# Performance work log

Measured on AMD Instinct MI355X. Metric: run time of the kernel, lower is better.

## Reference

```python
import jax, jax.numpy as jnp
import numpy as np
import math

EPS = 1e-5

def _ln(x, g, b):
    m = jnp.mean(x, axis=-1, keepdims=True)
    v = jnp.mean((x - m) ** 2, axis=-1, keepdims=True)
    return (x - m) * jax.lax.rsqrt(v + EPS) * g + b

def _heads(t, H):
    B, T, C = t.shape
    return t.reshape(B, T, H, C // H).transpose(0, 2, 1, 3)  # [B,H,T,D]

def _merge(t):
    B, H, T, D = t.shape
    return t.transpose(0, 2, 1, 3).reshape(B, T, H * D)

def _self_attn(x, w, b, pw, pb, H):
    B, T, C = x.shape
    q, k, v = jnp.split(x @ w + b, 3, axis=-1)
    q, k, v = _heads(q, H), _heads(k, H), _heads(v, H)
    D = C // H
    att = jnp.einsum('bhqd,bhkd->bhqk', q, k) * (1.0 / math.sqrt(D))
    causal = jnp.tril(jnp.ones((T, T), bool))
    att = jnp.where(causal[None, None], att, jnp.float32(-jnp.inf))
    att = jax.nn.softmax(att, axis=-1)
    out = _merge(jnp.einsum('bhqk,bhkd->bhqd', att, v))
    return out @ pw + pb

def _cross_attn(enc, dec, w, b, pw, pb, H):
    B, Td, C = dec.shape
    q_dec = jnp.split(dec @ w + b, 3, axis=-1)[0]
    _, k_enc, v_enc = jnp.split(enc @ w + b, 3, axis=-1)
    q = _heads(q_dec, H); k = _heads(k_enc, H); v = _heads(v_enc, H)
    D = C // H
    att = jnp.einsum('bhqd,bhkd->bhqk', q, k) * (1.0 / math.sqrt(D))
    att = jax.nn.softmax(att, axis=-1)
    out = _merge(jnp.einsum('bhqk,bhkd->bhqd', att, v))
    return out @ pw + pb

def _block(x, encoder_embd,
           ln1_g, ln1_b, ln2_g, ln2_b, ln3_g, ln3_b,
           attn_w, attn_b, aproj_w, aproj_b,
           ca_w, ca_b, caproj_w, caproj_b,
           fc_w, fc_b, mproj_w, mproj_b,
           down_w, down_b, up_w, up_b, H=16):
    x = x + _self_attn(_ln(x, ln1_g, ln1_b), attn_w, attn_b, aproj_w, aproj_b, H)
    x = x + _cross_attn(encoder_embd, _ln(x, ln2_g, ln2_b), ca_w, ca_b, caproj_w, caproj_b, H)
    h = jax.nn.gelu(_ln(x, ln3_g, ln3_b) @ fc_w + fc_b, approximate=True) @ mproj_w + mproj_b
    adapt = jax.nn.gelu(h @ down_w + down_b, approximate=True) @ up_w + up_b + h  # Adapter residual
    return x + adapt


def setup_inputs() -> dict:
    key = jax.random.key(0)
    ks = jax.random.split(key, 12)
    B, T, Te, C, H = 4, 1024, 257, 1024, 16
    s = 0.02
    f32 = jnp.float32
    return {
        'x': jax.random.normal(ks[0], (B, T, C), f32),
        'encoder_embd': jax.random.normal(ks[1], (B, Te, C), f32),
        'prefix_embd': jnp.zeros((B, 1, C), f32),
        'ln1_g': jnp.ones((C,), f32), 'ln1_b': jnp.zeros((C,), f32),
        'ln2_g': jnp.ones((C,), f32), 'ln2_b': jnp.zeros((C,), f32),
        'ln3_g': jnp.ones((C,), f32), 'ln3_b': jnp.zeros((C,), f32),
        'attn_w': jax.random.normal(ks[2], (C, 3 * C), f32) * s,
        'attn_b': jnp.zeros((3 * C,), f32),
        'aproj_w': jax.random.normal(ks[3], (C, C), f32) * s,
        'aproj_b': jnp.zeros((C,), f32),
        'ca_w': jax.random.normal(ks[4], (C, 3 * C), f32) * s,
        'ca_b': jnp.zeros((3 * C,), f32),
        'caproj_w': jax.random.normal(ks[5], (C, C), f32) * s,
        'caproj_b': jnp.zeros((C,), f32),
        'fc_w': jax.random.normal(ks[6], (C, 4 * C), f32) * s,
        'fc_b': jnp.zeros((4 * C,), f32),
        'mproj_w': jax.random.normal(ks[7], (4 * C, C), f32) * s,
        'mproj_b': jnp.zeros((C,), f32),
        'down_w': jax.random.normal(ks[8], (C, C // 4), f32) * s,
        'down_b': jnp.zeros((C // 4,), f32),
        'up_w': jax.random.normal(ks[9], (C // 4, C), f32) * s,
        'up_b': jnp.zeros((C,), f32),
    }


def reference(x, encoder_embd, prefix_embd,
              ln1_g, ln1_b, ln2_g, ln2_b, ln3_g, ln3_b,
              attn_w, attn_b, aproj_w, aproj_b,
              ca_w, ca_b, caproj_w, caproj_b,
              fc_w, fc_b, mproj_w, mproj_b,
              down_w, down_b, up_w, up_b):
    # prefix_embd unused (peft='adapter')
    return _block(x, encoder_embd,
                  ln1_g, ln1_b, ln2_g, ln2_b, ln3_g, ln3_b,
                  attn_w, attn_b, aproj_w, aproj_b,
                  ca_w, ca_b, caproj_w, caproj_b,
                  fc_w, fc_b, mproj_w, mproj_b,
                  down_w, down_b, up_w, up_b)
```

## Files before the change

### kernel.cpp

```cpp
#include <hip/hip_runtime.h>

typedef __attribute__((ext_vector_type(8))) short short8v;
typedef __attribute__((ext_vector_type(8))) unsigned short ushort8v;
typedef __attribute__((ext_vector_type(4))) float f32x4;

__device__ __forceinline__ unsigned short f2b(float f) {
  unsigned int u = __float_as_uint(f);
  unsigned int r = (u + 0x7FFFu + ((u >> 16) & 1u)) >> 16;
  return (unsigned short)r;
}
__device__ __forceinline__ float b2f(unsigned short h) {
  return __uint_as_float(((unsigned int)h) << 16);
}
__device__ __forceinline__ float gelu_f(float x) {
  float z = 0.7978845608028654f * (x + 0.044715f * x * x * x);
  float e = __expf(2.0f * z);
  float t = 1.0f - 2.0f / (e + 1.0f);
  return 0.5f * x * (1.0f + t);
}
__device__ __forceinline__ void gload16(const void* g, void* l) {
  __builtin_amdgcn_global_load_lds((const __attribute__((address_space(1))) unsigned int*)g,
                                   (__attribute__((address_space(3))) unsigned int*)l,
                                   16, 0, 0);
}

__global__ __launch_bounds__(256) void k_transpose_cvt(const float* __restrict__ w,
                                                       unsigned short* __restrict__ wt,
                                                       int K, int N) {
  __shared__ float tile[64][65];
  int tn = blockIdx.x * 64, tk = blockIdx.y * 64;
  int c = threadIdx.x & 63, r0 = threadIdx.x >> 6;
#pragma unroll
  for (int p = 0; p < 16; ++p) {
    int r = r0 + p * 4;
    tile[r][c] = w[(size_t)(tk + r) * N + tn + c];
  }
  __syncthreads();
#pragma unroll
  for (int p = 0; p < 16; ++p) {
    int r = r0 + p * 4;
    wt[(size_t)(tn + r) * K + tk + c] = f2b(tile[c][r]);
  }
}

__global__ void k_cvt_bf16(const float* __restrict__ in, unsigned short* __restrict__ out, int n) {
  int i = blockIdx.x * 256 + threadIdx.x;
  if (i < n) out[i] = f2b(in[i]);
}

__global__ __launch_bounds__(256) void k_ln(const float* __restrict__ in,
                                            const float* __restrict__ g,
                                            const float* __restrict__ b,
                                            unsigned short* __restrict__ out) {
  int row = blockIdx.x;
  const float* x = in + (size_t)row * 1024;
  int t = threadIdx.x;
  float v0 = x[t], v1 = x[t + 256], v2 = x[t + 512], v3 = x[t + 768];
  float s = v0 + v1 + v2 + v3;
  float s2 = v0 * v0 + v1 * v1 + v2 * v2 + v3 * v3;
#pragma unroll
  for (int m = 1; m < 64; m <<= 1) { s += __shfl_xor(s, m); s2 += __shfl_xor(s2, m); }
  __shared__ float rs[4], rs2[4];
  int w = t >> 6;
  if ((t & 63) == 0) { rs[w] = s; rs2[w] = s2; }
  __syncthreads();
  s = rs[0] + rs[1] + rs[2] + rs[3];
  s2 = rs2[0] + rs2[1] + rs2[2] + rs2[3];
  float mean = s * (1.0f / 1024.0f);
  float var = s2 * (1.0f / 1024.0f) - mean * mean;
  float rinv = rsqrtf(var + 1e-5f);
  unsigned short* o = out + (size_t)row * 1024;
  o[t]       = f2b((v0 - mean) * rinv * g[t]       + b[t]);
  o[t + 256] = f2b((v1 - mean) * rinv * g[t + 256] + b[t + 256]);
  o[t + 512] = f2b((v2 - mean) * rinv * g[t + 512] + b[t + 512]);
  o[t + 768] = f2b((v3 - mean) * rinv * g[t + 768] + b[t + 768]);
}

template <bool GELU, bool WF32, bool WBF16, int NRES>
__global__ __launch_bounds__(256) void k_gemm(const unsigned short* __restrict__ A,
                                              const unsigned short* __restrict__ W,
                                              const float* __restrict__ bias,
                                              const float* __restrict__ res1,
                                              const float* __restrict__ res2,
                                              float* __restrict__ outF,
                                              unsigned short* __restrict__ outB,
                                              int M, int N, int K) {
  __shared__ unsigned short sm[2][8192];
  int t = threadIdx.x;
  int tile_n = blockIdx.x * 128, tile_m = blockIdx.y * 128;
  int lane = t & 63, w = t >> 6;
  int wm = (w >> 1) * 64, wn = (w & 1) * 64;
  int lr = lane & 15;
  int kc = lane >> 4;

  int row0 = t >> 2, row1 = 64 + (t >> 2);
  int s0 = t & 3;
  int colA0 = (s0 ^ ((row0 >> 1) & 3)) * 8;
  int colA1 = (s0 ^ ((row1 >> 1) & 3)) * 8;
  int grA0 = tile_m + row0; if (grA0 >= M) grA0 = M - 1;
  int grA1 = tile_m + row1; if (grA1 >= M) grA1 = M - 1;
  const unsigned short* gA0 = A + (size_t)grA0 * K + colA0;
  const unsigned short* gA1 = A + (size_t)grA1 * K + colA1;
  const unsigned short* gB0 = W + (size_t)(tile_n + row0) * K + colA0;
  const unsigned short* gB1 = W + (size_t)(tile_n + row1) * K + colA1;

  f32x4 acc[4][4];
#pragma unroll
  for (int i = 0; i < 4; ++i)
#pragma unroll
    for (int j = 0; j < 4; ++j) acc[i][j] = f32x4{0.f, 0.f, 0.f, 0.f};

  int nsteps = K >> 5;
  gload16(gA0, &sm[0][t * 8]);
  gload16(gA1, &sm[0][2048 + t * 8]);
  gload16(gB0, &sm[0][4096 + t * 8]);
  gload16(gB1, &sm[0][6144 + t * 8]);

  for (int ks = 0; ks < nsteps; ++ks) {
    int cur = ks & 1, nxt = cur ^ 1;
    if (ks + 1 < nsteps) {
      int off = (ks + 1) << 5;
      gload16(gA0 + off, &sm[nxt][t * 8]);
      gload16(gA1 + off, &sm[nxt][2048 + t * 8]);
      gload16(gB0 + off, &sm[nxt][4096 + t * 8]);
      gload16(gB1 + off, &sm[nxt][6144 + t * 8]);
      asm volatile("s_waitcnt vmcnt(4)" ::: "memory");
    } else {
      asm volatile("s_waitcnt vmcnt(0)" ::: "memory");
    }
    __builtin_amdgcn_s_barrier();
    asm volatile("" ::: "memory");
    const unsigned short* buf = &sm[cur][0];
    short8v af[4], bfr[4];
#pragma unroll
    for (int i = 0; i < 4; ++i) {
      int rA = wm + i * 16 + lr;
      int sl = (kc ^ ((rA >> 1) & 3)) * 8;
      af[i] = *(const short8v*)&buf[rA * 32 + sl];
    }
#pragma unroll
    for (int j = 0; j < 4; ++j) {
      int rB = wn + j * 16 + lr;
      int sl = (kc ^ ((rB >> 1) & 3)) * 8;
      bfr[j] = *(const short8v*)&buf[4096 + rB * 32 + sl];
    }
#pragma unroll
    for (int i = 0; i < 4; ++i)
#pragma unroll
      for (int j = 0; j < 4; ++j)
        acc[i][j] = __builtin_amdgcn_mfma_f32_16x16x32_bf16(af[i], bfr[j], acc[i][j], 0, 0, 0);
    asm volatile("" ::: "memory");
    __builtin_amdgcn_s_barrier();
  }

  int r0 = (lane >> 4) * 4;
#pragma unroll
  for (int i = 0; i < 4; ++i) {
#pragma unroll
    for (int j = 0; j < 4; ++j) {
      int col = tile_n + wn + j * 16 + lr;
      float bv = bias[col];
#pragma unroll
      for (int q = 0; q < 4; ++q) {
        int row = tile_m + wm + i * 16 + r0 + q;
        if (row < M) {
          float v = acc[i][j][q] + bv;
          if (GELU) v = gelu_f(v);
          size_t o = (size_t)row * N + col;
          if (NRES >= 1) v += res1[o];
          if (NRES >= 2) v += res2[o];
          if (WF32) outF[o] = v;
          if (WBF16) outB[o] = f2b(v);
        }
      }
    }
  }
}

__global__ __launch_bounds__(256) void k_vtrans(const unsigned short* __restrict__ src,
                                                int src_stride, int src_off, int TB,
                                                unsigned short* __restrict__ dst, int dst_tstride) {
  __shared__ unsigned short tile[64][72];
  int tb = blockIdx.x, bh = blockIdx.y;
  int b = bh >> 4, h = bh & 15;
  int t = threadIdx.x;
  int r = t >> 2, c0 = (t & 3) * 16;
  int tok = tb * 64 + r; if (tok >= TB) tok = TB - 1;
  const unsigned short* s = src + (size_t)(b * TB + tok) * src_stride + src_off + h * 64 + c0;
  *(ushort8v*)&tile[r][c0] = *(const ushort8v*)s;
  *(ushort8v*)&tile[r][c0 + 8] = *(const ushort8v*)(s + 8);
  __syncthreads();
  unsigned short tmp[16];
#pragma unroll
  for (int j = 0; j < 16; ++j) tmp[j] = tile[c0 + j][r];
  unsigned short* dp = dst + ((size_t)bh * 64 + r) * dst_tstride + tb * 64 + c0;
  *(ushort8v*)dp = *(const ushort8v*)&tmp[0];
  *(ushort8v*)(dp + 8) = *(const ushort8v*)&tmp[8];
}

template <bool CAUSAL>
__global__ __launch_bounds__(256) void k_attn(
    const unsigned short* __restrict__ Qb, int q_stride,
    const unsigned short* __restrict__ Kb, int k_stride, int k_off, int TKR,
    const unsigned short* __restrict__ Vt, int vt_tstride,
    unsigned short* __restrict__ out, int Tk) {
  __shared__ unsigned short Kl[64 * 72];
  __shared__ unsigned short Vl[64 * 72];
  __shared__ unsigned short Pl[4][16 * 72];
  int qb = blockIdx.x, bh = blockIdx.y;
  int b = bh >> 4, h = bh & 15;
  int t = threadIdx.x, lane = t & 63, w = t >> 6;
  int g = lane >> 4, lc = lane & 15;

  int qrow_g = qb * 64 + w * 16 + lc;
  const unsigned short* qp = Qb + (size_t)(b * 1024 + qrow_g) * q_stride + h * 64 + g * 8;
  short8v aq0 = *(const short8v*)qp;
  short8v aq1 = *(const short8v*)(qp + 32);

  f32x4 o[4];
  float m_[4], l_[4];
#pragma unroll
  for (int dt = 0; dt < 4; ++dt) o[dt] = f32x4{0.f, 0.f, 0.f, 0.f};
#pragma unroll
  for (int r = 0; r < 4; ++r) { m_[r] = -3.0e38f; l_[r] = 0.0f; }

  int srow = t >> 2;
  int sc = (t & 3) * 16;
  int ntiles = CAUSAL ? (qb + 1) : ((Tk + 63) >> 6);

  for (int kt = 0; kt < ntiles; ++kt) {
    __syncthreads();
    {
      int kg = kt * 64 + srow;
      if (!CAUSAL && kg >= Tk) kg = Tk - 1;
      const unsigned short* ks = Kb + (size_t)(b * TKR + kg) * k_stride + k_off + h * 64 + sc;
      *(ushort8v*)&Kl[srow * 72 + sc]     = *(const ushort8v*)ks;
      *(ushort8v*)&Kl[srow * 72 + sc + 8] = *(const ushort8v*)(ks + 8);
      const unsigned short* vs = Vt + ((size_t)bh * 64 + srow) * vt_tstride + kt * 64 + sc;
      *(ushort8v*)&Vl[srow * 72 + sc]     = *(const ushort8v*)vs;
      *(ushort8v*)&Vl[srow * 72 + sc + 8] = *(const ushort8v*)(vs + 8);
    }
    __syncthreads();

    f32x4 s[4];
#pragma unroll
    for (int jt = 0; jt < 4; ++jt) {
      short8v bk0 = *(const short8v*)&Kl[(jt * 16 + lc) * 72 + g * 8];
      short8v bk1 = *(const short8v*)&Kl[(jt * 16 + lc) * 72 + g * 8 + 32];
      f32x4 acc = f32x4{0.f, 0.f, 0.f, 0.f};
      acc = __builtin_amdgcn_mfma_f32_16x16x32_bf16(aq0, bk0, acc, 0, 0, 0);
      acc = __builtin_amdgcn_mfma_f32_16x16x32_bf16(aq1, bk1, acc, 0, 0, 0);
      s[jt] = acc;
    }
#pragma unroll
    for (int jt = 0; jt < 4; ++jt)
#pragma unroll
      for (int r = 0; r < 4; ++r) {
        float sv = s[jt][r] * 0.125f;
        bool masked = CAUSAL ? (kt == qb && (jt * 16 + lc) > (w * 16 + g * 4 + r))
                             : (kt * 64 + jt * 16 + lc >= Tk);
        s[jt][r] = masked ? -3.0e38f : sv;
      }
    float f[4];
#pragma unroll
    for (int r = 0; r < 4; ++r) {
      float mx = fmaxf(fmaxf(s[0][r], s[1][r]), fmaxf(s[2][r], s[3][r]));
      mx = fmaxf(mx, __shfl_xor(mx, 1));
      mx = fmaxf(mx, __shfl_xor(mx, 2));
      mx = fmaxf(mx, __shfl_xor(mx, 4));
      mx = fmaxf(mx, __shfl_xor(mx, 8));
      float mnew = fmaxf(m_[r], mx);
      f[r] = __expf(m_[r] - mnew);
      m_[r] = mnew;
      float rsum = 0.0f;
#pragma unroll
      for (int jt = 0; jt < 4; ++jt) {
        float p = __expf(s[jt][r] - mnew);
        s[jt][r] = p;
        rsum += p;
      }
      rsum += __shfl_xor(rsum, 1);
      rsum += __shfl_xor(rsum, 2);
      rsum += __shfl_xor(rsum, 4);
      rsum += __shfl_xor(rsum, 8);
      l_[r] = l_[r] * f[r] + rsum;
    }
#pragma unroll
    for (int dt = 0; dt < 4; ++dt)
#pragma unroll
      for (int r = 0; r < 4; ++r) o[dt][r] *= f[r];
#pragma unroll
    for (int jt = 0; jt < 4; ++jt)
#pragma unroll
      for (int r = 0; r < 4; ++r)
        Pl[w][(g * 4 + r) * 72 + jt * 16 + lc] = f2b(s[jt][r]);
    short8v ap0 = *(const short8v*)&Pl[w][lc * 72 + g * 8];
    short8v ap1 = *(const short8v*)&Pl[w][lc * 72 + g * 8 + 32];
#pragma unroll
    for (int dt = 0; dt < 4; ++dt) {
      short8v bv0 = *(const short8v*)&Vl[(dt * 16 + lc) * 72 + g * 8];
      short8v bv1 = *(const short8v*)&Vl[(dt * 16 + lc) * 72 + g * 8 + 32];
      o[dt] = __builtin_amdgcn_mfma_f32_16x16x32_bf16(ap0, bv0, o[dt], 0, 0, 0);
      o[dt] = __builtin_amdgcn_mfma_f32_16x16x32_bf16(ap1, bv1, o[dt], 0, 0, 0);
    }
  }
  size_t orow = (size_t)(b * 1024 + qb * 64 + w * 16) * 1024 + h * 64;
#pragma unroll
  for (int r = 0; r < 4; ++r) {
    float inv = 1.0f / l_[r];
#pragma unroll
    for (int dt = 0; dt < 4; ++dt)
      out[orow + (size_t)(g * 4 + r) * 1024 + dt * 16 + lc] = f2b(o[dt][r] * inv);
  }
}

extern "C" void kernel_launch(void* const* d_in, const int* in_sizes, int n_in,
                              void* d_out, int out_size, void* d_ws, size_t ws_size,
                              hipStream_t stream) {
  (void)in_sizes; (void)n_in; (void)out_size; (void)ws_size;
  const float* x       = (const float*)d_in[0];
  const float* enc     = (const float*)d_in[1];
  const float* ln1_g   = (const float*)d_in[3];
  const float* ln1_b   = (const float*)d_in[4];
  const float* ln2_g   = (const float*)d_in[5];
  const float* ln2_b   = (const float*)d_in[6];
  const float* ln3_g   = (const float*)d_in[7];
  const float* ln3_b   = (const float*)d_in[8];
  const float* attn_w  = (const float*)d_in[9];
  const float* attn_b  = (const float*)d_in[10];
  const float* aproj_w = (const float*)d_in[11];
  const float* aproj_b = (const float*)d_in[12];
  const float* ca_w    = (const float*)d_in[13];
  const float* ca_b    = (const float*)d_in[14];
  const float* caproj_w= (const float*)d_in[15];
  const float* caproj_b= (const float*)d_in[16];
  const float* fc_w    = (const float*)d_in[17];
  const float* fc_b    = (const float*)d_in[18];
  const float* mproj_w = (const float*)d_in[19];
  const float* mproj_b = (const float*)d_in[20];
  const float* down_w  = (const float*)d_in[21];
  const float* down_b  = (const float*)d_in[22];
  const float* up_w    = (const float*)d_in[23];
  const float* up_b    = (const float*)d_in[24];
  float* out = (float*)d_out;
  char* ws = (char*)d_ws;

  const size_t O_WATTN = 0, O_WAPROJ = 6291456, O_WCA = 8388608, O_WCAPROJ = 14680064,
               O_WFC = 16777216, O_WMPROJ = 25165824, O_WDOWN = 33554432, O_WUP = 34078720,
               O_ENC = 34603008, O_LN = 36708352, O_BIG = 45096960,
               O_XRES = 78651392, O_HF = 95428608, O_ATTN = 112205824;

  unsigned short* wt_attn   = (unsigned short*)(ws + O_WATTN);
  unsigned short* wt_aproj  = (unsigned short*)(ws + O_WAPROJ);
  unsigned short* wt_ca     = (unsigned short*)(ws + O_WCA);
  unsigned short* wt_caproj = (unsigned short*)(ws + O_WCAPROJ);
  unsigned short* wt_fc     = (unsigned short*)(ws + O_WFC);
  unsigned short* wt_mproj  = (unsigned short*)(ws + O_WMPROJ);
  unsigned short* wt_down   = (unsigned short*)(ws + O_WDOWN);
  unsigned short* wt_up     = (unsigned short*)(ws + O_WUP);
  unsigned short* encbf     = (unsigned short*)(ws + O_ENC);
  unsigned short* lnout     = (unsigned short*)(ws + O_LN);
  unsigned short* hbf       = (unsigned short*)(ws + O_LN);
  unsigned short* qkvb      = (unsigned short*)(ws + O_BIG);
  unsigned short* vt_self   = (unsigned short*)(ws + O_BIG + 25165824);
  unsigned short* q2b       = (unsigned short*)(ws + O_BIG);
  unsigned short* kvb       = (unsigned short*)(ws + O_BIG + 8388608);
  unsigned short* vt_cross  = (unsigned short*)(ws + O_BIG + 12599296);
  unsigned short* caout     = (unsigned short*)(ws + O_BIG + 15220736);
  unsigned short* fcout     = (unsigned short*)(ws + O_BIG);
  float*          xres      = (float*)(ws + O_XRES);
  float*          hf        = (float*)(ws + O_HF);
  unsigned short* attnout   = (unsigned short*)(ws + O_ATTN);
  unsigned short* dmid      = (unsigned short*)(ws + O_ATTN);

  dim3 blk(256);

  k_transpose_cvt<<<dim3(48, 16), blk, 0, stream>>>(attn_w,  wt_attn,   1024, 3072);
  k_transpose_cvt<<<dim3(16, 16), blk, 0, stream>>>(aproj_w, wt_aproj,  1024, 1024);
  k_transpose_cvt<<<dim3(48, 16), blk, 0, stream>>>(ca_w,    wt_ca,     1024, 3072);
  k_transpose_cvt<<<dim3(16, 16), blk, 0, stream>>>(caproj_w,wt_caproj, 1024, 1024);
  k_transpose_cvt<<<dim3(64, 16), blk, 0, stream>>>(fc_w,    wt_fc,     1024, 4096);
  k_transpose_cvt<<<dim3(16, 64), blk, 0, stream>>>(mproj_w, wt_mproj,  4096, 1024);
  k_transpose_cvt<<<dim3(4, 16),  blk, 0, stream>>>(down_w,  wt_down,   1024, 256);
  k_transpose_cvt<<<dim3(16, 4),  blk, 0, stream>>>(up_w,    wt_up,     256,  1024);
  k_cvt_bf16<<<dim3(4112), blk, 0, stream>>>(enc, encbf, 1028 * 1024);

  k_ln<<<dim3(4096), blk, 0, stream>>>(x, ln1_g, ln1_b, lnout);
  k_gemm<false, false, true, 0><<<dim3(24, 32), blk, 0, stream>>>(
      lnout, wt_attn, attn_b, nullptr, nullptr, nullptr, qkvb, 4096, 3072, 1024);
  k_vtrans<<<dim3(16, 64), blk, 0, stream>>>(qkvb, 3072, 2048, 1024, vt_self, 1024);
  k_attn<true><<<dim3(16, 64), blk, 0, stream>>>(
      qkvb, 3072, qkvb, 3072, 1024, 1024, vt_self, 1024, attnout, 1024);
  k_gemm<false, true, false, 1><<<dim3(8, 32), blk, 0, stream>>>(
      attnout, wt_aproj, aproj_b, x, nullptr, xres, nullptr, 4096, 1024, 1024);

  k_ln<<<dim3(4096), blk, 0, stream>>>(xres, ln2_g, ln2_b, lnout);
  k_gemm<false, false, true, 0><<<dim3(8, 32), blk, 0, stream>>>(
      lnout, wt_ca, ca_b, nullptr, nullptr, nullptr, q2b, 4096, 1024, 1024);
  k_gemm<false, false, true, 0><<<dim3(16, 9), blk, 0, stream>>>(
      encbf, wt_ca + (size_t)1024 * 1024, ca_b + 1024, nullptr, nullptr, nullptr, kvb,
      1028, 2048, 1024);
  k_vtrans<<<dim3(5, 64), blk, 0, stream>>>(kvb, 2048, 1024, 257, vt_cross, 320);
  k_attn<false><<<dim3(16, 64), blk, 0, stream>>>(
      q2b, 1024, kvb, 2048, 0, 257, vt_cross, 320, caout, 257);
  k_gemm<false, true, false, 1><<<dim3(8, 32), blk, 0, stream>>>(
      caout, wt_caproj, caproj_b, xres, nullptr, xres, nullptr, 4096, 1024, 1024);

  k_ln<<<dim3(4096), blk, 0, stream>>>(xres, ln3_g, ln3_b, lnout);
  k_gemm<true, false, true, 0><<<dim3(32, 32), blk, 0, stream>>>(
      lnout, wt_fc, fc_b, nullptr, nullptr, nullptr, fcout, 4096, 4096, 1024);
  k_gemm<false, true, true, 0><<<dim3(8, 32), blk, 0, stream>>>(
      fcout, wt_mproj, mproj_b, nullptr, nullptr, hf, hbf, 4096, 1024, 4096);

  k_gemm<true, false, true, 0><<<dim3(2, 32), blk, 0, stream>>>(
      hbf, wt_down, down_b, nullptr, nullptr, nullptr, dmid, 4096, 256, 1024);
  k_gemm<false, true, false, 2><<<dim3(8, 32), blk, 0, stream>>>(
      dmid, wt_up, up_b, hf, xres, out, nullptr, 4096, 1024, 256);
}
```

Before: 473.9 us.

## Add 256x256-tile 8-wave GEMM with deep LDS pipeline and split-K for mproj

```diff
diff --git a/kernel.cpp b/kernel.cpp
--- a/kernel.cpp
+++ b/kernel.cpp
@@ -2,6 +2,7 @@
 
 typedef __attribute__((ext_vector_type(8))) short short8v;
 typedef __attribute__((ext_vector_type(8))) unsigned short ushort8v;
+typedef __attribute__((ext_vector_type(4))) unsigned short ushort4v;
 typedef __attribute__((ext_vector_type(4))) float f32x4;
 
 __device__ __forceinline__ unsigned short f2b(float f) {
@@ -74,6 +75,137 @@
   o[t + 256] = f2b((v1 - mean) * rinv * g[t + 256] + b[t + 256]);
   o[t + 512] = f2b((v2 - mean) * rinv * g[t + 512] + b[t + 512]);
   o[t + 768] = f2b((v3 - mean) * rinv * g[t + 768] + b[t + 768]);
+}
+
+template <bool GELU, bool BIAS, bool WF32, bool WBF16>
+__global__ __launch_bounds__(512, 2) void k_gemm256(
+    const unsigned short* __restrict__ A, int lda,
+    const unsigned short* __restrict__ W, int ldw,
+    const float* __restrict__ bias,
+    float* __restrict__ outF, unsigned short* __restrict__ outB, int ldo,
+    int K, size_t zA, size_t zW, size_t zO) {
+  __shared__ unsigned short lds[65536];
+  int t = threadIdx.x;
+  int bz = blockIdx.z;
+  A += (size_t)bz * zA;
+  W += (size_t)bz * zW;
+  if (WF32) outF += (size_t)bz * zO;
+  int tileM = blockIdx.y * 256, tileN = blockIdx.x * 256;
+  int lane = t & 63, w = t >> 6;
+  int wm = w >> 2, wn = w & 3;
+  int lr16 = lane & 15, kc4 = lane >> 4;
+
+  int row1 = t >> 2, cs1 = t & 3;
+  int row2 = row1 + 128;
+  int c1 = (cs1 ^ ((row1 >> 1) & 3)) * 8;
+  int c2 = (cs1 ^ ((row2 >> 1) & 3)) * 8;
+  const unsigned short* a1 = A + (size_t)(tileM + row1) * lda + c1;
+  const unsigned short* a2 = A + (size_t)(tileM + row2) * lda + c2;
+  const unsigned short* w1 = W + (size_t)(tileN + row1) * ldw + c1;
+  const unsigned short* w2 = W + (size_t)(tileN + row2) * ldw + c2;
+
+  f32x4 acc[8][4];
+#pragma unroll
+  for (int i = 0; i < 8; ++i)
+#pragma unroll
+    for (int j = 0; j < 4; ++j) acc[i][j] = f32x4{0.f, 0.f, 0.f, 0.f};
+
+  int ntiles = K >> 6;
+  int H = ntiles * 4;
+
+#define STAGE_HALF(h)                                                        \
+  do {                                                                       \
+    int tile_s = (h) >> 2, id = (h) & 3, slot = (h) & 7;                     \
+    int koff = tile_s * 64 + (id >> 1) * 32;                                 \
+    unsigned short* dst = &lds[slot * 8192 + t * 8];                         \
+    if (id & 1) { gload16(w1 + koff, dst); gload16(w2 + koff, dst + 4096); } \
+    else        { gload16(a1 + koff, dst); gload16(a2 + koff, dst + 4096); } \
+  } while (0)
+
+#pragma unroll
+  for (int h = 0; h < 6; ++h) STAGE_HALF(h);
+
+  for (int T = 0; T < ntiles; ++T) {
+    if (T == ntiles - 1) asm volatile("s_waitcnt vmcnt(0)" ::: "memory");
+    else                 asm volatile("s_waitcnt vmcnt(4)" ::: "memory");
+    __builtin_amdgcn_s_barrier();
+    asm volatile("" ::: "memory");
+    int abase = (T & 1) * 4 * 8192;
+    short8v bf_[4];
+#pragma unroll
+    for (int q = 0; q < 4; ++q) {
+      const int ks = q >> 1, mh = q & 1;
+      int aoff = abase + 2 * ks * 8192;
+      int boff = abase + (1 + 2 * ks) * 8192;
+      short8v af_[4];
+#pragma unroll
+      for (int m4 = 0; m4 < 4; ++m4) {
+        int row = wm * 128 + (mh * 4 + m4) * 16 + lr16;
+        af_[m4] = *(const short8v*)&lds[aoff + row * 32 + (kc4 ^ ((row >> 1) & 3)) * 8];
+      }
+      if (mh == 0) {
+#pragma unroll
+        for (int n = 0; n < 4; ++n) {
+          int row = wn * 64 + n * 16 + lr16;
+          bf_[n] = *(const short8v*)&lds[boff + row * 32 + (kc4 ^ ((row >> 1) & 3)) * 8];
+        }
+      }
+      int h = T * 4 + q + 6;
+      if (h < H) STAGE_HALF(h);
+      __builtin_amdgcn_s_barrier();
+      asm volatile("s_waitcnt lgkmcnt(0)" ::: "memory");
+      __builtin_amdgcn_sched_barrier(0);
+      __builtin_amdgcn_s_setprio(1);
+#pragma unroll
+      for (int m4 = 0; m4 < 4; ++m4)
+#pragma unroll
+        for (int n = 0; n < 4; ++n)
+          acc[mh * 4 + m4][n] =
+              __builtin_amdgcn_mfma_f32_16x16x32_bf16(af_[m4], bf_[n], acc[mh * 4 + m4][n], 0, 0, 0);
+      __builtin_amdgcn_s_setprio(0);
+      __builtin_amdgcn_sched_barrier(0);
+      __builtin_amdgcn_s_barrier();
+      asm volatile("" ::: "memory");
+    }
+  }
+#undef STAGE_HALF
+
+#pragma unroll
+  for (int mi = 0; mi < 8; ++mi) {
+#pragma unroll
+    for (int n = 0; n < 4; ++n) {
+      int col = tileN + wn * 64 + n * 16 + lr16;
+      float bv = BIAS ? bias[col] : 0.0f;
+#pragma unroll
+      for (int qi = 0; qi < 4; ++qi) {
+        int row = tileM + wm * 128 + mi * 16 + kc4 * 4 + qi;
+        float v = acc[mi][n][qi] + bv;
+        if (GELU) v = gelu_f(v);
+        size_t o = (size_t)row * ldo + col;
+        if (WF32) outF[o] = v;
+        if (WBF16) outB[o] = f2b(v);
+      }
+    }
+  }
+}
+
+__global__ __launch_bounds__(256) void k_red4(const float* __restrict__ p,
+                                              const float* __restrict__ bias,
+                                              float* __restrict__ hf,
+                                              unsigned short* __restrict__ hb) {
+  size_t i = ((size_t)blockIdx.x * 256 + threadIdx.x) * 4;
+  const size_t S = (size_t)4096 * 1024;
+  f32x4 v0 = *(const f32x4*)&p[i];
+  f32x4 v1 = *(const f32x4*)&p[i + S];
+  f32x4 v2 = *(const f32x4*)&p[i + 2 * S];
+  f32x4 v3 = *(const f32x4*)&p[i + 3 * S];
+  f32x4 bv = *(const f32x4*)&bias[i & 1023];
+  f32x4 v = v0 + v1 + v2 + v3 + bv;
+  *(f32x4*)&hf[i] = v;
+  ushort4v o;
+#pragma unroll
+  for (int j = 0; j < 4; ++j) o[j] = f2b(v[j]);
+  *(ushort4v*)&hb[i] = o;
 }
 
 template <bool GELU, bool WF32, bool WBF16, int NRES>
@@ -317,7 +449,7 @@
 extern "C" void kernel_launch(void* const* d_in, const int* in_sizes, int n_in,
                               void* d_out, int out_size, void* d_ws, size_t ws_size,
                               hipStream_t stream) {
-  (void)in_sizes; (void)n_in; (void)out_size; (void)ws_size;
+  (void)in_sizes; (void)n_in; (void)out_size;
   const float* x       = (const float*)d_in[0];
   const float* enc     = (const float*)d_in[1];
   const float* ln1_g   = (const float*)d_in[3];
@@ -348,7 +480,8 @@
   const size_t O_WATTN = 0, O_WAPROJ = 6291456, O_WCA = 8388608, O_WCAPROJ = 14680064,
                O_WFC = 16777216, O_WMPROJ = 25165824, O_WDOWN = 33554432, O_WUP = 34078720,
                O_ENC = 34603008, O_LN = 36708352, O_BIG = 45096960,
-               O_XRES = 78651392, O_HF = 95428608, O_ATTN = 112205824;
+               O_XRES = 78651392, O_HF = 95428608, O_ATTN = 112205824,
+               O_PART = 121634816;
 
   unsigned short* wt_attn   = (unsigned short*)(ws + O_WATTN);
   unsigned short* wt_aproj  = (unsigned short*)(ws + O_WAPROJ);
@@ -372,8 +505,12 @@
   float*          hf        = (float*)(ws + O_HF);
   unsigned short* attnout   = (unsigned short*)(ws + O_ATTN);
   unsigned short* dmid      = (unsigned short*)(ws + O_ATTN);
+  float*          part      = (float*)(ws + O_PART);
+
+  bool splitk = ws_size >= O_PART + 4ull * 4096 * 1024 * 4;
 
   dim3 blk(256);
+  dim3 blk5(512);
 
   k_transpose_cvt<<<dim3(48, 16), blk, 0, stream>>>(attn_w,  wt_attn,   1024, 3072);
   k_transpose_cvt<<<dim3(16, 16), blk, 0, stream>>>(aproj_w, wt_aproj,  1024, 1024);
@@ -386,8 +523,8 @@
   k_cvt_bf16<<<dim3(4112), blk, 0, stream>>>(enc, encbf, 1028 * 1024);
 
   k_ln<<<dim3(4096), blk, 0, stream>>>(x, ln1_g, ln1_b, lnout);
-  k_gemm<false, false, true, 0><<<dim3(24, 32), blk, 0, stream>>>(
-      lnout, wt_attn, attn_b, nullptr, nullptr, nullptr, qkvb, 4096, 3072, 1024);
+  k_gemm256<false, true, false, true><<<dim3(12, 16), blk5, 0, stream>>>(
+      lnout, 1024, wt_attn, 1024, attn_b, nullptr, qkvb, 3072, 1024, 0, 0, 0);
   k_vtrans<<<dim3(16, 64), blk, 0, stream>>>(qkvb, 3072, 2048, 1024, vt_self, 1024);
   k_attn<true><<<dim3(16, 64), blk, 0, stream>>>(
       qkvb, 3072, qkvb, 3072, 1024, 1024, vt_self, 1024, attnout, 1024);
@@ -407,10 +544,17 @@
       caout, wt_caproj, caproj_b, xres, nullptr, xres, nullptr, 4096, 1024, 1024);
 
   k_ln<<<dim3(4096), blk, 0, stream>>>(xres, ln3_g, ln3_b, lnout);
-  k_gemm<true, false, true, 0><<<dim3(32, 32), blk, 0, stream>>>(
-      lnout, wt_fc, fc_b, nullptr, nullptr, nullptr, fcout, 4096, 4096, 1024);
-  k_gemm<false, true, true, 0><<<dim3(8, 32), blk, 0, stream>>>(
-      fcout, wt_mproj, mproj_b, nullptr, nullptr, hf, hbf, 4096, 1024, 4096);
+  k_gemm256<true, true, false, true><<<dim3(16, 16), blk5, 0, stream>>>(
+      lnout, 1024, wt_fc, 1024, fc_b, nullptr, fcout, 4096, 1024, 0, 0, 0);
+  if (splitk) {
+    k_gemm256<false, false, true, false><<<dim3(4, 16, 4), blk5, 0, stream>>>(
+        fcout, 4096, wt_mproj, 4096, nullptr, part, nullptr, 1024, 1024,
+        1024, 1024, (size_t)4096 * 1024);
+    k_red4<<<dim3(4096), blk, 0, stream>>>(part, mproj_b, hf, hbf);
+  } else {
+    k_gemm<false, true, true, 0><<<dim3(8, 32), blk, 0, stream>>>(
+        fcout, wt_mproj, mproj_b, nullptr, nullptr, hf, hbf, 4096, 1024, 4096);
+  }
 
   k_gemm<true, false, true, 0><<<dim3(2, 32), blk, 0, stream>>>(
       hbf, wt_down, down_b, nullptr, nullptr, nullptr, dmid, 4096, 256, 1024);
```

Measured after the change: 532.5 us. 12.4% more time.
